# Optimization experiments

Measured on AMD Instinct MI355X. Metric: run time of the kernel, lower is better.

The kernel has to match this reference:

```python
import jax, jax.numpy as jnp
import numpy as np

D_K = 1024
HEADS = 16
HK = 64
HV = 64


def setup_inputs() -> dict:
    key = jax.random.key(0)
    ks = jax.random.split(key, 12)
    B, S = 4, 2048
    sc_in = 1.0 / np.sqrt(D_K)
    sc_u = 1.0 / np.sqrt(HV * HEADS)
    return {
        "q": jax.random.normal(ks[0], (B, S, D_K), jnp.float32),
        "k": jax.random.normal(ks[1], (B, S, D_K), jnp.float32),
        "v": jax.random.normal(ks[2], (B, S, D_K), jnp.float32),
        "Wq": jax.random.normal(ks[3], (D_K, HK * HEADS), jnp.float32) * sc_in,
        "bq": jax.random.normal(ks[4], (HK * HEADS,), jnp.float32) * sc_in,
        "Wk": jax.random.normal(ks[5], (D_K, HK * HEADS), jnp.float32) * sc_in,
        "bk": jax.random.normal(ks[6], (HK * HEADS,), jnp.float32) * sc_in,
        "Wv": jax.random.normal(ks[7], (D_K, HV * HEADS), jnp.float32) * sc_in,
        "bv": jax.random.normal(ks[8], (HV * HEADS,), jnp.float32) * sc_in,
        "Wu": jax.random.normal(ks[9], (HV * HEADS, D_K), jnp.float32) * sc_u,
        "bu": jax.random.normal(ks[10], (D_K,), jnp.float32) * sc_u,
    }


def reference(q, k, v, Wq, bq, Wk, bk, Wv, bv, Wu, bu):
    B, S, _ = q.shape
    # QKV projections, split heads: (B, S, H, dh) -> (B, H, S, dh)
    qh = (q @ Wq + bq).reshape(B, S, HEADS, HK).transpose(0, 2, 1, 3)
    kh = (k @ Wk + bk).reshape(B, S, HEADS, HK).transpose(0, 2, 1, 3)
    vh = (v @ Wv + bv).reshape(B, S, HEADS, HV).transpose(0, 2, 1, 3)
    # Naive attention: scores scaled by sqrt(head_size) as in Sdpa
    scores = jnp.einsum("bhqd,bhkd->bhqk", qh, kh) / jnp.sqrt(
        jnp.asarray(HK, qh.dtype)
    )
    attn = jax.nn.softmax(scores, axis=-1)
    out = jnp.einsum("bhqk,bhkd->bhqd", attn, vh)  # (B, H, S, HV)
    # Merge heads: (B, S, H*HV), then output projection
    merged = out.transpose(0, 2, 1, 3).reshape(B, S, HEADS * HV)
    return merged @ Wu + bu
```

## Files before the change

kernel.cpp:

```cpp
#include <hip/hip_runtime.h>

typedef __bf16 bf16;
typedef __bf16 bf16x8 __attribute__((ext_vector_type(8)));
typedef __bf16 bf16x4 __attribute__((ext_vector_type(4)));
typedef float  f32x4  __attribute__((ext_vector_type(4)));
typedef short  s16x4  __attribute__((ext_vector_type(4)));

#define GLD_LDS16(gp, lp) __builtin_amdgcn_global_load_lds( \
    (const __attribute__((address_space(1))) unsigned int*)(const void*)(gp), \
    (__attribute__((address_space(3))) unsigned int*)(void*)(lp), 16, 0, 0)

static __device__ __forceinline__ f32x4 mfma16(bf16x4 a, bf16x4 b, f32x4 c) {
    return __builtin_amdgcn_mfma_f32_16x16x16bf16_1k(
        __builtin_bit_cast(s16x4, a), __builtin_bit_cast(s16x4, b), c, 0, 0, 0);
}

constexpr int BB = 4, SSEQ = 2048, DK = 1024, NH = 16, DH = 64;
constexpr int M = BB * SSEQ;

constexpr size_t SZ_X = (size_t)M * DK * 2;
constexpr size_t SZ_W = (size_t)DK * DK * 2;
constexpr size_t OFF_QBF = 0;
constexpr size_t OFF_KBF = OFF_QBF + SZ_X;
constexpr size_t OFF_VBF = OFF_KBF + SZ_X;
constexpr size_t OFF_WQT = OFF_VBF + SZ_X;
constexpr size_t OFF_WKT = OFF_WQT + SZ_W;
constexpr size_t OFF_WVT = OFF_WKT + SZ_W;
constexpr size_t OFF_WUT = OFF_WVT + SZ_W;
constexpr size_t OFF_QH  = OFF_WUT + SZ_W;
constexpr size_t OFF_KH  = OFF_QH + SZ_X;
constexpr size_t OFF_VTH = OFF_KH + SZ_X;
constexpr size_t OFF_MRG = OFF_VTH + SZ_X;

__global__ void cvt_x(const float* __restrict__ q, const float* __restrict__ k,
                      const float* __restrict__ v,
                      bf16* __restrict__ qb, bf16* __restrict__ kb, bf16* __restrict__ vb) {
    const float* s = (blockIdx.z == 0) ? q : (blockIdx.z == 1) ? k : v;
    bf16*        d = (blockIdx.z == 0) ? qb : (blockIdx.z == 1) ? kb : vb;
    size_t i = (size_t)blockIdx.x * blockDim.x + threadIdx.x;
    float4 val = ((const float4*)s)[i];
    bf16x4 o = { (bf16)val.x, (bf16)val.y, (bf16)val.z, (bf16)val.w };
    ((bf16x4*)d)[i] = o;
}

__global__ void cvt_wT(const float* __restrict__ wq, const float* __restrict__ wk,
                       const float* __restrict__ wv, const float* __restrict__ wu,
                       bf16* __restrict__ wqt, bf16* __restrict__ wkt,
                       bf16* __restrict__ wvt, bf16* __restrict__ wut) {
    const float* w = (blockIdx.z == 0) ? wq : (blockIdx.z == 1) ? wk
                   : (blockIdx.z == 2) ? wv : wu;
    bf16* o        = (blockIdx.z == 0) ? wqt : (blockIdx.z == 1) ? wkt
                   : (blockIdx.z == 2) ? wvt : wut;
    __shared__ float t[64][65];
    int tx = threadIdx.x & 63, ty = threadIdx.x >> 6;
    int bx = blockIdx.x * 64, by = blockIdx.y * 64;
#pragma unroll
    for (int r = 0; r < 16; r++) {
        int row = ty * 16 + r;
        t[row][tx] = w[(size_t)(by + row) * DK + bx + tx];
    }
    __syncthreads();
#pragma unroll
    for (int r = 0; r < 16; r++) {
        int row2 = ty * 16 + r;
        o[(size_t)(bx + row2) * DK + by + tx] = (bf16)t[tx][row2];
    }
}

struct GArg {
    const bf16* A; const bf16* BT; const float* bias; void* out; int mode; float oscale;
};

__global__ __launch_bounds__(256, 2) void gemm_bt(GArg g0, GArg g1, GArg g2) {
    GArg g;
    if (blockIdx.z == 0) g = g0; else if (blockIdx.z == 1) g = g1; else g = g2;
    __shared__ __attribute__((aligned(16))) bf16 As[128 * 32];
    __shared__ __attribute__((aligned(16))) bf16 Bs[128 * 32];
    const int tid = threadIdx.x;
    const int lane = tid & 63, wv = tid >> 6;
    const int wm = (wv & 1) * 64, wn = (wv >> 1) * 64;
    const int cl = lane & 15, qd = lane >> 4;
    const int rowbase = blockIdx.y * 128, colbase = blockIdx.x * 128;

    f32x4 acc[4][4];
#pragma unroll
    for (int i = 0; i < 4; i++)
#pragma unroll
        for (int j = 0; j < 4; j++) acc[i][j] = f32x4{0.f, 0.f, 0.f, 0.f};

    const bool swapped = (g.mode == 1);
    for (int k0 = 0; k0 < DK; k0 += 32) {
        __syncthreads();
#pragma unroll
        for (int c = 0; c < 2; c++) {
            int f = (c * 256 + tid) * 8;
            int row = f >> 5, col = f & 31;
            GLD_LDS16(g.A + (size_t)(rowbase + row) * DK + k0 + col, &As[f]);
        }
#pragma unroll
        for (int c = 0; c < 2; c++) {
            int f = (c * 256 + tid) * 8;
            int row = f >> 5, col = f & 31;
            GLD_LDS16(g.BT + (size_t)(colbase + row) * DK + k0 + col, &Bs[f]);
        }
        __syncthreads();
        bf16x8 af[4], bfr[4];
#pragma unroll
        for (int i = 0; i < 4; i++)
            af[i] = *(const bf16x8*)&As[(wm + i * 16 + cl) * 32 + qd * 8];
#pragma unroll
        for (int j = 0; j < 4; j++)
            bfr[j] = *(const bf16x8*)&Bs[(wn + j * 16 + cl) * 32 + qd * 8];
        if (swapped) {
#pragma unroll
            for (int i = 0; i < 4; i++)
#pragma unroll
                for (int j = 0; j < 4; j++)
                    acc[i][j] = __builtin_amdgcn_mfma_f32_16x16x32_bf16(bfr[j], af[i], acc[i][j], 0, 0, 0);
        } else {
#pragma unroll
            for (int i = 0; i < 4; i++)
#pragma unroll
                for (int j = 0; j < 4; j++)
                    acc[i][j] = __builtin_amdgcn_mfma_f32_16x16x32_bf16(af[i], bfr[j], acc[i][j], 0, 0, 0);
        }
    }

    if (g.mode == 2) {
        float* out = (float*)g.out;
#pragma unroll
        for (int i = 0; i < 4; i++)
#pragma unroll
            for (int j = 0; j < 4; j++)
#pragma unroll
                for (int r = 0; r < 4; r++) {
                    int row = rowbase + wm + i * 16 + qd * 4 + r;
                    int col = colbase + wn + j * 16 + cl;
                    out[(size_t)row * DK + col] = (acc[i][j][r] + g.bias[col]) * g.oscale;
                }
    } else if (g.mode == 0) {
        bf16* out = (bf16*)g.out;
#pragma unroll
        for (int i = 0; i < 4; i++)
#pragma unroll
            for (int j = 0; j < 4; j++)
#pragma unroll
                for (int r = 0; r < 4; r++) {
                    int row = rowbase + wm + i * 16 + qd * 4 + r;
                    int col = colbase + wn + j * 16 + cl;
                    float v = (acc[i][j][r] + g.bias[col]) * g.oscale;
                    out[(size_t)row * DK + col] = (bf16)v;
                }
    } else {
        bf16* out = (bf16*)g.out;
#pragma unroll
        for (int i = 0; i < 4; i++)
#pragma unroll
            for (int j = 0; j < 4; j++)
#pragma unroll
                for (int r = 0; r < 4; r++) {
                    int colg = colbase + wn + j * 16 + qd * 4 + r;
                    int rowg = rowbase + wm + i * 16 + cl;
                    int b_ = rowg >> 11, s_ = rowg & 2047;
                    float v = (acc[i][j][r] + g.bias[colg]) * g.oscale;
                    out[((size_t)(b_ * NH + (colg >> 6)) * DH + (colg & 63)) * SSEQ + s_] = (bf16)v;
                }
    }
}

__global__ __launch_bounds__(256, 4) void attn(const bf16* __restrict__ Qh,
                                               const bf16* __restrict__ Kh,
                                               const bf16* __restrict__ VTh,
                                               bf16* __restrict__ mrg) {
    __shared__ __attribute__((aligned(16))) bf16 Ks[2][64 * 64];
    __shared__ __attribute__((aligned(16))) bf16 VTs[2][64 * 64];
    const int tid = threadIdx.x;
    const int lane = tid & 63, w = tid >> 6;
    const int cl = lane & 15, qd = lane >> 4;
    const int F = blockIdx.x;
    const int xcd = F & 7, slot = F >> 3;
    const int bh = xcd * 8 + (slot & 7);
    const int qt = slot >> 3;
    const int b_ = bh >> 4, h_ = bh & 15;
    const int qbase = qt * 128;
    const bf16* Qb = Qh + ((size_t)b_ * SSEQ) * DK + h_ * DH;
    const bf16* Kb = Kh + ((size_t)b_ * SSEQ) * DK + h_ * DH;
    const bf16* Vb = VTh + (size_t)bh * DH * SSEQ;

    bf16x8 qf[2][2];
#pragma unroll
    for (int mi = 0; mi < 2; mi++) {
        int q = qbase + w * 32 + mi * 16 + cl;
        qf[mi][0] = *(const bf16x8*)&Qb[(size_t)q * DK + qd * 8];
        qf[mi][1] = *(const bf16x8*)&Qb[(size_t)q * DK + 32 + qd * 8];
    }
    f32x4 O[2][4];
#pragma unroll
    for (int mi = 0; mi < 2; mi++)
#pragma unroll
        for (int jv = 0; jv < 4; jv++) O[mi][jv] = f32x4{0.f, 0.f, 0.f, 0.f};
    float ps[2] = {0.f, 0.f};

    auto stage = [&](int kt, int buf) {
#pragma unroll
        for (int c = 0; c < 2; c++) {
            int L = c * 256 + tid;
            int row = L >> 3, lc = (L & 7) ^ (row & 7);
            GLD_LDS16(Kb + (size_t)(kt * 64 + row) * DK + lc * 8, &Ks[buf][L * 8]);
        }
#pragma unroll
        for (int c = 0; c < 2; c++) {
            int L = c * 256 + tid;
            int row = L >> 3, lc = (L & 7) ^ (row & 7);
            GLD_LDS16(Vb + (size_t)row * SSEQ + kt * 64 + lc * 8, &VTs[buf][L * 8]);
        }
    };
    stage(0, 0);

    for (int kt = 0; kt < 32; kt++) {
        const int buf = kt & 1;
        __syncthreads();
        if (kt + 1 < 32) stage(kt + 1, buf ^ 1);

        bf16x4 pf[2][4];
#pragma unroll
        for (int jt = 0; jt < 4; jt++) {
            bf16x8 kf0 = *(const bf16x8*)&Ks[buf][(jt * 16 + cl) * 64 + ((qd ^ (cl & 7)) * 8)];
            bf16x8 kf1 = *(const bf16x8*)&Ks[buf][(jt * 16 + cl) * 64 + (((4 + qd) ^ (cl & 7)) * 8)];
#pragma unroll
            for (int mi = 0; mi < 2; mi++) {
                f32x4 S = __builtin_amdgcn_mfma_f32_16x16x32_bf16(kf0, qf[mi][0],
                                                                  f32x4{0.f, 0.f, 0.f, 0.f}, 0, 0, 0);
                S = __builtin_amdgcn_mfma_f32_16x16x32_bf16(kf1, qf[mi][1], S, 0, 0, 0);
                bf16x4 p4;
                float s = 0.f;
#pragma unroll
                for (int r = 0; r < 4; r++) {
                    float p = __builtin_amdgcn_exp2f(S[r]);
                    s += p;
                    p4[r] = (bf16)p;
                }
                ps[mi] += s;
                pf[mi][jt] = p4;
            }
        }

#pragma unroll
        for (int jt = 0; jt < 4; jt++) {
#pragma unroll
            for (int jv = 0; jv < 4; jv++) {
                bf16x4 vf = *(const bf16x4*)&VTs[buf][(jv * 16 + cl) * 64 +
                                (((jt * 2 + (qd >> 1)) ^ (cl & 7)) * 8) + (qd & 1) * 4];
#pragma unroll
                for (int mi = 0; mi < 2; mi++)
                    O[mi][jv] = mfma16(vf, pf[mi][jt], O[mi][jv]);
            }
        }
    }

#pragma unroll
    for (int mi = 0; mi < 2; mi++) {
        float t = ps[mi];
        t += __shfl_xor(t, 16);
        t += __shfl_xor(t, 32);
        float inv = 1.0f / t;
        int q = qbase + w * 32 + mi * 16 + cl;
        size_t ro = ((size_t)(b_ * SSEQ + q)) * DK + h_ * DH;
#pragma unroll
        for (int jv = 0; jv < 4; jv++) {
            bf16x4 o4;
#pragma unroll
            for (int r = 0; r < 4; r++) o4[r] = (bf16)(O[mi][jv][r] * inv);
            *(bf16x4*)&mrg[ro + jv * 16 + qd * 4] = o4;
        }
    }
}

extern "C" void kernel_launch(void* const* d_in, const int* in_sizes, int n_in,
                              void* d_out, int out_size, void* d_ws, size_t ws_size,
                              hipStream_t stream) {
    const float* q  = (const float*)d_in[0];
    const float* k  = (const float*)d_in[1];
    const float* v  = (const float*)d_in[2];
    const float* Wq = (const float*)d_in[3];
    const float* bq = (const float*)d_in[4];
    const float* Wk = (const float*)d_in[5];
    const float* bk = (const float*)d_in[6];
    const float* Wv = (const float*)d_in[7];
    const float* bv = (const float*)d_in[8];
    const float* Wu = (const float*)d_in[9];
    const float* bu = (const float*)d_in[10];
    char* ws = (char*)d_ws;
    bf16* qbf = (bf16*)(ws + OFF_QBF);
    bf16* kbf = (bf16*)(ws + OFF_KBF);
    bf16* vbf = (bf16*)(ws + OFF_VBF);
    bf16* wqt = (bf16*)(ws + OFF_WQT);
    bf16* wkt = (bf16*)(ws + OFF_WKT);
    bf16* wvt = (bf16*)(ws + OFF_WVT);
    bf16* wut = (bf16*)(ws + OFF_WUT);
    bf16* qh  = (bf16*)(ws + OFF_QH);
    bf16* kh  = (bf16*)(ws + OFF_KH);
    bf16* vth = (bf16*)(ws + OFF_VTH);
    bf16* mrg = (bf16*)(ws + OFF_MRG);

    cvt_x<<<dim3(8192, 1, 3), 256, 0, stream>>>(q, k, v, qbf, kbf, vbf);
    cvt_wT<<<dim3(16, 16, 4), 256, 0, stream>>>(Wq, Wk, Wv, Wu, wqt, wkt, wvt, wut);

    GArg gq{qbf, wqt, bq, (void*)qh, 0, 0.18033688011112043f};
    GArg gk{kbf, wkt, bk, (void*)kh, 0, 1.0f};
    GArg gv{vbf, wvt, bv, (void*)vth, 1, 1.0f};
    gemm_bt<<<dim3(8, 64, 3), 256, 0, stream>>>(gq, gk, gv);

    attn<<<dim3(1024), 256, 0, stream>>>(qh, kh, vth, mrg);

    GArg go{mrg, wut, bu, d_out, 2, 1.0f};
    gemm_bt<<<dim3(8, 64, 1), 256, 0, stream>>>(go, go, go);
}
```

Measured before the change: 362.4 us.

## Fuse fp32-to-bf16 input conversion into QKV GEMM and compute softmax sum via MFMA

Removes the separate cvt_x kernel. The QKV GEMM now loads fp32 activations into registers, converts them to bf16 and stores them into LDS, prefetching the next K-slice during compute. This avoids writing and re-reading three bf16 copies of the inputs. The attention kernel replaces the scalar row-sum of exp values with an extra MFMA against a ones vector, and the output GEMM becomes a specialized kernel; the cost is more register pressure and a synchronous LDS store path for A instead of direct global-to-LDS loads.

```diff
diff --git a/kernel.cpp b/kernel.cpp
--- a/kernel.cpp
+++ b/kernel.cpp
@@ -20,10 +20,7 @@
 
 constexpr size_t SZ_X = (size_t)M * DK * 2;
 constexpr size_t SZ_W = (size_t)DK * DK * 2;
-constexpr size_t OFF_QBF = 0;
-constexpr size_t OFF_KBF = OFF_QBF + SZ_X;
-constexpr size_t OFF_VBF = OFF_KBF + SZ_X;
-constexpr size_t OFF_WQT = OFF_VBF + SZ_X;
+constexpr size_t OFF_WQT = 0;
 constexpr size_t OFF_WKT = OFF_WQT + SZ_W;
 constexpr size_t OFF_WVT = OFF_WKT + SZ_W;
 constexpr size_t OFF_WUT = OFF_WVT + SZ_W;
@@ -31,17 +28,6 @@
 constexpr size_t OFF_KH  = OFF_QH + SZ_X;
 constexpr size_t OFF_VTH = OFF_KH + SZ_X;
 constexpr size_t OFF_MRG = OFF_VTH + SZ_X;
-
-__global__ void cvt_x(const float* __restrict__ q, const float* __restrict__ k,
-                      const float* __restrict__ v,
-                      bf16* __restrict__ qb, bf16* __restrict__ kb, bf16* __restrict__ vb) {
-    const float* s = (blockIdx.z == 0) ? q : (blockIdx.z == 1) ? k : v;
-    bf16*        d = (blockIdx.z == 0) ? qb : (blockIdx.z == 1) ? kb : vb;
-    size_t i = (size_t)blockIdx.x * blockDim.x + threadIdx.x;
-    float4 val = ((const float4*)s)[i];
-    bf16x4 o = { (bf16)val.x, (bf16)val.y, (bf16)val.z, (bf16)val.w };
-    ((bf16x4*)d)[i] = o;
-}
 
 __global__ void cvt_wT(const float* __restrict__ wq, const float* __restrict__ wk,
                        const float* __restrict__ wv, const float* __restrict__ wu,
@@ -67,12 +53,12 @@
     }
 }
 
-struct GArg {
-    const bf16* A; const bf16* BT; const float* bias; void* out; int mode; float oscale;
+struct QArg {
+    const float* A; const bf16* BT; const float* bias; bf16* out; int mode; float oscale;
 };
 
-__global__ __launch_bounds__(256, 2) void gemm_bt(GArg g0, GArg g1, GArg g2) {
-    GArg g;
+__global__ __launch_bounds__(256, 2) void gemm_qkv(QArg g0, QArg g1, QArg g2) {
+    QArg g;
     if (blockIdx.z == 0) g = g0; else if (blockIdx.z == 1) g = g1; else g = g2;
     __shared__ __attribute__((aligned(16))) bf16 As[128 * 32];
     __shared__ __attribute__((aligned(16))) bf16 Bs[128 * 32];
@@ -88,22 +74,38 @@
 #pragma unroll
         for (int j = 0; j < 4; j++) acc[i][j] = f32x4{0.f, 0.f, 0.f, 0.f};
 
+    float4 areg[2][2];
+    auto preloadA = [&](int k0) {
+#pragma unroll
+        for (int c = 0; c < 2; c++) {
+            int f = (c * 256 + tid) * 8;
+            const float* p = g.A + (size_t)(rowbase + (f >> 5)) * DK + k0 + (f & 31);
+            areg[c][0] = ((const float4*)p)[0];
+            areg[c][1] = ((const float4*)p)[1];
+        }
+    };
+    preloadA(0);
+
     const bool swapped = (g.mode == 1);
     for (int k0 = 0; k0 < DK; k0 += 32) {
         __syncthreads();
 #pragma unroll
         for (int c = 0; c < 2; c++) {
             int f = (c * 256 + tid) * 8;
-            int row = f >> 5, col = f & 31;
-            GLD_LDS16(g.A + (size_t)(rowbase + row) * DK + k0 + col, &As[f]);
-        }
-#pragma unroll
-        for (int c = 0; c < 2; c++) {
-            int f = (c * 256 + tid) * 8;
-            int row = f >> 5, col = f & 31;
-            GLD_LDS16(g.BT + (size_t)(colbase + row) * DK + k0 + col, &Bs[f]);
-        }
-        __syncthreads();
+            GLD_LDS16(g.BT + (size_t)(colbase + (f >> 5)) * DK + k0 + (f & 31), &Bs[f]);
+        }
+#pragma unroll
+        for (int c = 0; c < 2; c++) {
+            int f = (c * 256 + tid) * 8;
+            bf16x8 cv;
+            cv[0] = (bf16)areg[c][0].x; cv[1] = (bf16)areg[c][0].y;
+            cv[2] = (bf16)areg[c][0].z; cv[3] = (bf16)areg[c][0].w;
+            cv[4] = (bf16)areg[c][1].x; cv[5] = (bf16)areg[c][1].y;
+            cv[6] = (bf16)areg[c][1].z; cv[7] = (bf16)areg[c][1].w;
+            *(bf16x8*)&As[f] = cv;
+        }
+        __syncthreads();
+        if (k0 + 32 < DK) preloadA(k0 + 32);
         bf16x8 af[4], bfr[4];
 #pragma unroll
         for (int i = 0; i < 4; i++)
@@ -126,20 +128,8 @@
         }
     }
 
-    if (g.mode == 2) {
-        float* out = (float*)g.out;
-#pragma unroll
-        for (int i = 0; i < 4; i++)
-#pragma unroll
-            for (int j = 0; j < 4; j++)
-#pragma unroll
-                for (int r = 0; r < 4; r++) {
-                    int row = rowbase + wm + i * 16 + qd * 4 + r;
-                    int col = colbase + wn + j * 16 + cl;
-                    out[(size_t)row * DK + col] = (acc[i][j][r] + g.bias[col]) * g.oscale;
-                }
-    } else if (g.mode == 0) {
-        bf16* out = (bf16*)g.out;
+    if (g.mode == 0) {
+        bf16* out = g.out;
 #pragma unroll
         for (int i = 0; i < 4; i++)
 #pragma unroll
@@ -152,7 +142,7 @@
                     out[(size_t)row * DK + col] = (bf16)v;
                 }
     } else {
-        bf16* out = (bf16*)g.out;
+        bf16* out = g.out;
 #pragma unroll
         for (int i = 0; i < 4; i++)
 #pragma unroll
@@ -166,6 +156,63 @@
                     out[((size_t)(b_ * NH + (colg >> 6)) * DH + (colg & 63)) * SSEQ + s_] = (bf16)v;
                 }
     }
+}
+
+__global__ __launch_bounds__(256, 2) void gemm_out(const bf16* __restrict__ A,
+                                                   const bf16* __restrict__ BT,
+                                                   const float* __restrict__ bias,
+                                                   float* __restrict__ out) {
+    __shared__ __attribute__((aligned(16))) bf16 As[128 * 32];
+    __shared__ __attribute__((aligned(16))) bf16 Bs[128 * 32];
+    const int tid = threadIdx.x;
+    const int lane = tid & 63, wv = tid >> 6;
+    const int wm = (wv & 1) * 64, wn = (wv >> 1) * 64;
+    const int cl = lane & 15, qd = lane >> 4;
+    const int rowbase = blockIdx.y * 128, colbase = blockIdx.x * 128;
+
+    f32x4 acc[4][4];
+#pragma unroll
+    for (int i = 0; i < 4; i++)
+#pragma unroll
+        for (int j = 0; j < 4; j++) acc[i][j] = f32x4{0.f, 0.f, 0.f, 0.f};
+
+    for (int k0 = 0; k0 < DK; k0 += 32) {
+        __syncthreads();
+#pragma unroll
+        for (int c = 0; c < 2; c++) {
+            int f = (c * 256 + tid) * 8;
+            GLD_LDS16(A + (size_t)(rowbase + (f >> 5)) * DK + k0 + (f & 31), &As[f]);
+        }
+#pragma unroll
+        for (int c = 0; c < 2; c++) {
+            int f = (c * 256 + tid) * 8;
+            GLD_LDS16(BT + (size_t)(colbase + (f >> 5)) * DK + k0 + (f & 31), &Bs[f]);
+        }
+        __syncthreads();
+        bf16x8 af[4], bfr[4];
+#pragma unroll
+        for (int i = 0; i < 4; i++)
+            af[i] = *(const bf16x8*)&As[(wm + i * 16 + cl) * 32 + qd * 8];
+#pragma unroll
+        for (int j = 0; j < 4; j++)
+            bfr[j] = *(const bf16x8*)&Bs[(wn + j * 16 + cl) * 32 + qd * 8];
+#pragma unroll
+        for (int i = 0; i < 4; i++)
+#pragma unroll
+            for (int j = 0; j < 4; j++)
+                acc[i][j] = __builtin_amdgcn_mfma_f32_16x16x32_bf16(af[i], bfr[j], acc[i][j], 0, 0, 0);
+    }
+
+#pragma unroll
+    for (int i = 0; i < 4; i++)
+#pragma unroll
+        for (int j = 0; j < 4; j++)
+#pragma unroll
+            for (int r = 0; r < 4; r++) {
+                int row = rowbase + wm + i * 16 + qd * 4 + r;
+                int col = colbase + wn + j * 16 + cl;
+                out[(size_t)row * DK + col] = acc[i][j][r] + bias[col];
+            }
 }
 
 __global__ __launch_bounds__(256, 4) void attn(const bf16* __restrict__ Qh,
@@ -199,7 +246,9 @@
     for (int mi = 0; mi < 2; mi++)
 #pragma unroll
         for (int jv = 0; jv < 4; jv++) O[mi][jv] = f32x4{0.f, 0.f, 0.f, 0.f};
-    float ps[2] = {0.f, 0.f};
+    f32x4 Lacc[2] = {f32x4{0.f, 0.f, 0.f, 0.f}, f32x4{0.f, 0.f, 0.f, 0.f}};
+    const bf16x4 vones = (cl == 0) ? bf16x4{(bf16)1.f, (bf16)1.f, (bf16)1.f, (bf16)1.f}
+                                   : bf16x4{(bf16)0.f, (bf16)0.f, (bf16)0.f, (bf16)0.f};
 
     auto stage = [&](int kt, int buf) {
 #pragma unroll
@@ -217,8 +266,7 @@
     };
     stage(0, 0);
 
-    for (int kt = 0; kt < 32; kt++) {
-        const int buf = kt & 1;
+    auto body = [&](int kt, int buf) {
         __syncthreads();
         if (kt + 1 < 32) stage(kt + 1, buf ^ 1);
 
@@ -233,14 +281,9 @@
                                                                   f32x4{0.f, 0.f, 0.f, 0.f}, 0, 0, 0);
                 S = __builtin_amdgcn_mfma_f32_16x16x32_bf16(kf1, qf[mi][1], S, 0, 0, 0);
                 bf16x4 p4;
-                float s = 0.f;
-#pragma unroll
-                for (int r = 0; r < 4; r++) {
-                    float p = __builtin_amdgcn_exp2f(S[r]);
-                    s += p;
-                    p4[r] = (bf16)p;
-                }
-                ps[mi] += s;
+#pragma unroll
+                for (int r = 0; r < 4; r++)
+                    p4[r] = (bf16)__builtin_amdgcn_exp2f(S[r]);
                 pf[mi][jt] = p4;
             }
         }
@@ -255,15 +298,20 @@
                 for (int mi = 0; mi < 2; mi++)
                     O[mi][jv] = mfma16(vf, pf[mi][jt], O[mi][jv]);
             }
-        }
+#pragma unroll
+            for (int mi = 0; mi < 2; mi++)
+                Lacc[mi] = mfma16(vones, pf[mi][jt], Lacc[mi]);
+        }
+    };
+    for (int kt = 0; kt < 32; kt += 2) {
+        body(kt, 0);
+        body(kt + 1, 1);
     }
 
 #pragma unroll
     for (int mi = 0; mi < 2; mi++) {
-        float t = ps[mi];
-        t += __shfl_xor(t, 16);
-        t += __shfl_xor(t, 32);
-        float inv = 1.0f / t;
+        float l = __shfl(Lacc[mi][0], cl);
+        float inv = 1.0f / l;
         int q = qbase + w * 32 + mi * 16 + cl;
         size_t ro = ((size_t)(b_ * SSEQ + q)) * DK + h_ * DH;
 #pragma unroll
@@ -291,9 +339,6 @@
     const float* Wu = (const float*)d_in[9];
     const float* bu = (const float*)d_in[10];
     char* ws = (char*)d_ws;
-    bf16* qbf = (bf16*)(ws + OFF_QBF);
-    bf16* kbf = (bf16*)(ws + OFF_KBF);
-    bf16* vbf = (bf16*)(ws + OFF_VBF);
     bf16* wqt = (bf16*)(ws + OFF_WQT);
     bf16* wkt = (bf16*)(ws + OFF_WKT);
     bf16* wvt = (bf16*)(ws + OFF_WVT);
@@ -303,16 +348,14 @@
     bf16* vth = (bf16*)(ws + OFF_VTH);
     bf16* mrg = (bf16*)(ws + OFF_MRG);
 
-    cvt_x<<<dim3(8192, 1, 3), 256, 0, stream>>>(q, k, v, qbf, kbf, vbf);
     cvt_wT<<<dim3(16, 16, 4), 256, 0, stream>>>(Wq, Wk, Wv, Wu, wqt, wkt, wvt, wut);
 
-    GArg gq{qbf, wqt, bq, (void*)qh, 0, 0.18033688011112043f};
-    GArg gk{kbf, wkt, bk, (void*)kh, 0, 1.0f};
-    GArg gv{vbf, wvt, bv, (void*)vth, 1, 1.0f};
-    gemm_bt<<<dim3(8, 64, 3), 256, 0, stream>>>(gq, gk, gv);
+    QArg gq{q, wqt, bq, qh, 0, 0.18033688011112043f};
+    QArg gk{k, wkt, bk, kh, 0, 1.0f};
+    QArg gv{v, wvt, bv, vth, 1, 1.0f};
+    gemm_qkv<<<dim3(8, 64, 3), 256, 0, stream>>>(gq, gk, gv);
 
     attn<<<dim3(1024), 256, 0, stream>>>(qh, kh, vth, mrg);
 
-    GArg go{mrg, wut, bu, d_out, 2, 1.0f};
-    gemm_bt<<<dim3(8, 64, 1), 256, 0, stream>>>(go, go, go);
-}
+    gemm_out<<<dim3(8, 64), 256, 0, stream>>>(mrg, wut, bu, (float*)d_out);
+}
```

Measured after the change: 375.3 us. 1.04x slower.
